# Optimization experiments

Measured on AMD Instinct MI355X. Metric: run time of the kernel, lower is better.

## Reference

```python
import jax, jax.numpy as jnp
import numpy as np

THR = 10.0           # spike threshold (all layers, igarss2023 config)
LEAK1, LEAK2, LEAK3 = 9.0, 1.0, 0.0  # subtractive leak per layer
POOL1_K, POOL1_S = 7, 6
POOL2_K, POOL2_S = 2, 2
WTA_BLOCK = 2        # local spatial WTA window


def conv2d_same(x, w):
    # x: (B,C,H,W), w: (O,I,kh,kw)
    return jax.lax.conv_general_dilated(
        x, w, window_strides=(1, 1), padding='SAME',
        dimension_numbers=('NCHW', 'OIHW', 'NCHW'))


def maxpool(x, k, s):
    return jax.lax.reduce_window(
        x, -jnp.inf, jax.lax.max, (1, 1, k, k), (1, 1, s, s), 'VALID')


def wta(mem, spk, block=WTA_BLOCK):
    """Winner-take-all lateral inhibition ('both' mode):
    (1) channel competition: only the channel with max membrane at each
        spatial location may spike; (2) local spatial competition: only the
        max-membrane neuron within each block x block window of each map
        may spike. Requires H,W divisible by block."""
    C = mem.shape[1]
    ch_win = jnp.argmax(mem, axis=1)                         # (B,H,W)
    ch_mask = jax.nn.one_hot(ch_win, C, axis=1, dtype=mem.dtype)  # (B,C,H,W)
    loc = jax.lax.reduce_window(
        mem, -jnp.inf, jax.lax.max,
        (1, 1, block, block), (1, 1, block, block), 'VALID')
    loc_up = jnp.repeat(jnp.repeat(loc, block, axis=2), block, axis=3)
    sp_mask = (mem >= loc_up).astype(mem.dtype)
    return spk * ch_mask * sp_mask


def lif_step(mem, inp, leak, use_wta):
    # integrate -> threshold -> WTA -> reset-to-zero -> subtractive leak
    mem = mem + inp
    spk = (mem >= THR).astype(mem.dtype)
    if use_wta:
        spk = wta(mem, spk)
    mem = jnp.where(spk > 0, 0.0, mem)
    mem = jnp.maximum(mem - leak, 0.0)
    return mem, spk


def setup_inputs() -> dict:
    key = jax.random.key(0)
    k0, k1, k2, k3 = jax.random.split(key, 4)
    T, B, H, W = 20, 8, 256, 256
    x = jax.random.uniform(k0, (T, B, 1, H, W), dtype=jnp.float32)
    # STDP-style weights are non-negative in [0,1)
    w1 = jax.random.uniform(k1, (4, 1, 5, 5), dtype=jnp.float32)
    w2 = jax.random.uniform(k2, (36, 4, 5, 5), dtype=jnp.float32)
    w3 = jax.random.uniform(k3, (1, 36, 7, 7), dtype=jnp.float32)
    return {"x": x, "w1": w1, "w2": w2, "w3": w3}


def reference(x, w1, w2, w3):
    T, B, _, H, W = x.shape
    H1, W1 = H, W                                   # conv1 SAME
    H2 = (H1 - POOL1_K) // POOL1_S + 1              # 42
    W2 = (W1 - POOL1_K) // POOL1_S + 1
    H3 = (H2 - POOL2_K) // POOL2_S + 1              # 21
    W3 = (W2 - POOL2_K) // POOL2_S + 1
    C1, C2, C3 = w1.shape[0], w2.shape[0], w3.shape[0]

    m1_0 = jnp.zeros((B, C1, H1, W1), x.dtype)
    m2_0 = jnp.zeros((B, C2, H2, W2), x.dtype)
    m3_0 = jnp.zeros((B, C3, H3, W3), x.dtype)

    def step(carry, xt):
        m1, m2, m3 = carry
        m1, s1 = lif_step(m1, conv2d_same(xt, w1), LEAK1, True)
        p1 = maxpool(s1, POOL1_K, POOL1_S)
        m2, s2 = lif_step(m2, conv2d_same(p1, w2), LEAK2, True)
        p2 = maxpool(s2, POOL2_K, POOL2_S)
        m3, s3 = lif_step(m3, conv2d_same(p2, w3), LEAK3, False)
        return (m1, m2, m3), s3

    _, cls_spikes = jax.lax.scan(step, (m1_0, m2_0, m3_0), x)
    return cls_spikes  # (T, B, n_classes, H3, W3)
```

## Files before the change

### kernel.cpp

```cpp
#include <hip/hip_runtime.h>
#include <stdint.h>

#define THR 10.0f
#define AGT __HIP_MEMORY_SCOPE_AGENT

static constexpr size_t OFF_P2  = 2097152;
static constexpr size_t OFF_BAR = 2359296;

static __device__ __forceinline__ uint32_t ldu32(const uint32_t* p) {
    return __hip_atomic_load(p, __ATOMIC_RELAXED, AGT);
}
static __device__ __forceinline__ void stu32(uint32_t* p, uint32_t v) {
    __hip_atomic_store(p, v, __ATOMIC_RELAXED, AGT);
}
static __device__ __forceinline__ void stu16(uint16_t* p, uint16_t v) {
    __hip_atomic_store(p, v, __ATOMIC_RELAXED, AGT);
}
static __device__ __forceinline__ uint32_t rmwread(uint32_t* p) {
    return __hip_atomic_fetch_add(p, 0u, __ATOMIC_RELAXED, AGT);
}

__global__ __launch_bounds__(256) void zero_bar(uint32_t* __restrict__ bar) {
    if (threadIdx.x < 256) bar[threadIdx.x] = 0u;
}

__device__ __forceinline__ void gbar(uint32_t* bar, int bid, uint32_t n) {
    __syncthreads();
    if (threadIdx.x == 0) {
        uint32_t* base = bar + (bid >> 6) * 32;
        uint32_t a = __hip_atomic_fetch_add(base, 1u, __ATOMIC_RELAXED, AGT);
        if (a == 64u * n - 1u)
            __hip_atomic_fetch_add(base + 16, 1u, __ATOMIC_RELAXED, AGT);
        while (rmwread(base + 16) < n)
            __builtin_amdgcn_s_sleep(2);
    }
    __syncthreads();
}

__global__ __launch_bounds__(256, 2) void spike_persist(
    const float* __restrict__ x,
    const float* __restrict__ w1,
    const float* __restrict__ w2,
    const float* __restrict__ w3,
    float* __restrict__ out,
    uint8_t* __restrict__ s1b,
    uint8_t* __restrict__ p2b,
    uint32_t* __restrict__ bar)
{
    __shared__ union {
        float    xs[2112];
        uint32_t st32[527];
    } u;
    __shared__ float    ps[400];
    __shared__ float    mem_s[1296];
    __shared__ float    bm_s[324];
    __shared__ int      wc_s[36];
    __shared__ uint32_t p2a[18];

    const int tid = threadIdx.x;
    const int bid = blockIdx.x;
    uint32_t nbar = 0;

    const int b1 = bid >> 6;
    const int r0 = (bid & 63) * 4;
    const int tr = tid >> 7, tc = tid & 127;

    const int tIdx = bid & 63;
    const int b2 = bid >> 6;
    const int tyi = tIdx >> 3, txi = tIdx & 7;
    const int oy2 = tyi < 5 ? 6 * tyi : 30 + 4 * (tyi - 5);
    const int ox2 = txi < 5 ? 6 * txi : 30 + 4 * (txi - 5);
    const int th2 = tyi < 5 ? 6 : 4;
    const int tw2 = txi < 5 ? 6 : 4;
    const int wave = tid >> 6, lane = tid & 63;
    const int pr = lane / 6, pc = lane - 6 * pr;
    const bool act = (pr < th2) && (pc < tw2);
    const int prA = pr > 5 ? 0 : pr, pcA = pc;

    const int lid3 = (bid & 63) * 4 + wave;
    const int kyl = lane / 7, kxl = lane % 7;

    float w3v[36];
#pragma unroll
    for (int c = 0; c < 36; c++) w3v[c] = (lane < 49) ? w3[c * 49 + lane] : 0.f;

    int aoff[9]; bool aval[9];
#pragma unroll
    for (int i = 0; i < 9; i++) {
        int idx = tid + i * 256;
        int row = idx / 264, col = idx - row * 264;
        int gy = r0 + row - 2, gx = col - 2;
        aval[i] = (idx < 2112) && gy >= 0 && gy < 256 && gx >= 0 && gx < 256;
        aoff[i] = gy * 256 + gx;
    }
    const size_t s1soff = ((size_t)(b1 * 128 + (r0 >> 1) + tr)) * 128 + tc;

    const int rb0 = 3 * oy2 - 6;
    const int cb0 = (3 * ox2 - 6) >> 1;
    int boff[3]; bool bval[3];
#pragma unroll
    for (int i = 0; i < 3; i++) {
        int idx = tid + i * 256;
        int row = idx / 17, w = idx - row * 17;
        int grow = rb0 + row, gcol = cb0 + w;
        bval[i] = (idx < 527) && grow >= 0 && grow < 128 && gcol >= 0 && gcol < 64;
        boff[i] = (b2 * 128 + grow) * 64 + gcol;
    }

    bool l3in[2], l3v[2]; int l3o[2];
#pragma unroll
    for (int rep = 0; rep < 2; rep++) {
        int o = lid3 + rep * 256;
        int rr = o / 21, cl = o - rr * 21;
        int yy = rr + kyl - 3, xx = cl + kxl - 3;
        l3in[rep] = o < 441;
        l3v[rep] = (o < 441) && (lane < 49) && yy >= 0 && yy < 21 && xx >= 0 && xx < 21;
        l3o[rep] = (b2 * 441 + yy * 21 + xx) << 1;
    }

    float m1r[4][2][2];
#pragma unroll
    for (int c = 0; c < 4; c++)
#pragma unroll
        for (int dy = 0; dy < 2; dy++)
#pragma unroll
            for (int dx = 0; dx < 2; dx++) m1r[c][dy][dx] = 0.f;
    float m2r[9];
#pragma unroll
    for (int i = 0; i < 9; i++) m2r[i] = 0.f;
    float m3r[2] = {0.f, 0.f};

    for (int k = 0; k < 7; k++) {
        uint32_t pfB[4][3];
#pragma unroll
        for (int tt = 0; tt < 4; tt++) {
            int tb = 4 * k - 4 + tt;
            if (tb >= 0 && tb < 20) {
                const uint32_t* s1r32 = reinterpret_cast<const uint32_t*>(
                    s1b + (size_t)(tb & 7) * 262144);
#pragma unroll
                for (int i = 0; i < 3; i++)
                    pfB[tt][i] = bval[i] ? ldu32(s1r32 + boff[i]) : 0u;
            }
        }
        uint32_t pfLlo[4][2], pfLhi[4][2];
#pragma unroll
        for (int tt = 0; tt < 4; tt++) {
            int tl = 4 * k - 8 + tt;
            if (tl >= 0 && tl < 20) {
                const uint32_t* pb32 = reinterpret_cast<const uint32_t*>(
                    p2b + (size_t)(tl & 7) * 32768);
#pragma unroll
                for (int rep = 0; rep < 2; rep++) {
                    pfLlo[tt][rep] = l3v[rep] ? ldu32(pb32 + l3o[rep]) : 0u;
                    pfLhi[tt][rep] = l3v[rep] ? ldu32(pb32 + l3o[rep] + 1) : 0u;
                }
            }
        }

#pragma unroll
        for (int tt = 0; tt < 4; tt++) {
            const int t = 4 * k + tt;
            if (t < 20) {
                uint16_t* s1w = reinterpret_cast<uint16_t*>(s1b + (size_t)(t & 7) * 262144);
                const float* xb = x + ((size_t)t * 8 + b1) * 65536;
                __syncthreads();
#pragma unroll
                for (int i = 0; i < 9; i++) {
                    int idx = tid + i * 256;
                    if (idx < 2112) u.xs[idx] = aval[i] ? xb[aoff[i]] : 0.f;
                }
                __syncthreads();

                const float2* xs2 = reinterpret_cast<const float2*>(u.xs);
                float p[6][6];
#pragma unroll
                for (int i = 0; i < 6; i++)
#pragma unroll
                    for (int j = 0; j < 3; j++) {
                        float2 v = xs2[(2 * tr + i) * 132 + tc + j];
                        p[i][2 * j] = v.x; p[i][2 * j + 1] = v.y;
                    }

                float acc[4][2][2];
#pragma unroll
                for (int c = 0; c < 4; c++)
#pragma unroll
                    for (int dy = 0; dy < 2; dy++)
#pragma unroll
                        for (int dx = 0; dx < 2; dx++) acc[c][dy][dx] = 0.f;
#pragma unroll
                for (int c = 0; c < 4; c++)
#pragma unroll
                    for (int ky = 0; ky < 5; ky++)
#pragma unroll
                        for (int kx = 0; kx < 5; kx++) {
                            float w = w1[c * 25 + ky * 5 + kx];
#pragma unroll
                            for (int dy = 0; dy < 2; dy++)
#pragma unroll
                                for (int dx = 0; dx < 2; dx++)
                                    acc[c][dy][dx] = fmaf(p[dy + ky][dx + kx], w, acc[c][dy][dx]);
                        }

                float mem[4][2][2];
#pragma unroll
                for (int c = 0; c < 4; c++)
#pragma unroll
                    for (int dy = 0; dy < 2; dy++)
#pragma unroll
                        for (int dx = 0; dx < 2; dx++)
                            mem[c][dy][dx] = m1r[c][dy][dx] + acc[c][dy][dx];

                int wc[2][2];
#pragma unroll
                for (int dy = 0; dy < 2; dy++)
#pragma unroll
                    for (int dx = 0; dx < 2; dx++) {
                        int w = 0; float mx = mem[0][dy][dx];
#pragma unroll
                        for (int c = 1; c < 4; c++) {
                            float v = mem[c][dy][dx];
                            if (v > mx) { mx = v; w = c; }
                        }
                        wc[dy][dx] = w;
                    }

                float bm[4];
#pragma unroll
                for (int c = 0; c < 4; c++)
                    bm[c] = fmaxf(fmaxf(mem[c][0][0], mem[c][0][1]),
                                  fmaxf(mem[c][1][0], mem[c][1][1]));

                uint32_t bits = 0;
#pragma unroll
                for (int c = 0; c < 4; c++)
#pragma unroll
                    for (int dy = 0; dy < 2; dy++)
#pragma unroll
                        for (int dx = 0; dx < 2; dx++) {
                            float m = mem[c][dy][dx];
                            bool s = (m >= THR) && (wc[dy][dx] == c) && (m >= bm[c]);
                            m1r[c][dy][dx] = fmaxf((s ? 0.f : m) - 9.0f, 0.f);
                            bits |= (s ? 1u : 0u) << (c * 4 + dy * 2 + dx);
                        }
                stu16(reinterpret_cast<uint16_t*>(s1w) + s1soff, (uint16_t)bits);
            }
        }

#pragma unroll
        for (int tt = 0; tt < 4; tt++) {
            const int tl = 4 * k - 8 + tt;
            if (tl >= 0 && tl < 20) {
#pragma unroll
                for (int rep = 0; rep < 2; rep++) {
                    if (l3in[rep]) {
                        int o = lid3 + rep * 256;
                        uint32_t lo = pfLlo[tt][rep], hi = pfLhi[tt][rep];
                        float accv = 0.f;
#pragma unroll
                        for (int c = 0; c < 32; c++) accv += ((lo >> c) & 1u) ? w3v[c] : 0.f;
#pragma unroll
                        for (int c = 0; c < 4; c++)  accv += ((hi >> c) & 1u) ? w3v[32 + c] : 0.f;
#pragma unroll
                        for (int off = 32; off; off >>= 1) accv += __shfl_xor(accv, off, 64);
                        float memv3 = m3r[rep] + accv;
                        bool s = memv3 >= THR;
                        if (lane == 0) out[(size_t)tl * 3528 + b2 * 441 + o] = s ? 1.f : 0.f;
                        m3r[rep] = fmaxf(s ? 0.f : memv3, 0.f);
                    }
                }
            }
        }

#pragma unroll
        for (int tt = 0; tt < 4; tt++) {
            const int tb = 4 * k - 4 + tt;
            if (tb >= 0 && tb < 20) {
                uint32_t* p2w32 = reinterpret_cast<uint32_t*>(p2b + (size_t)(tb & 7) * 32768);

                __syncthreads();
#pragma unroll
                for (int i = 0; i < 3; i++) {
                    int idx = tid + i * 256;
                    if (idx < 527) u.st32[idx] = pfB[tt][i];
                }
                __syncthreads();

                if (tid < 100) {
                    int r = tid / 10, cc2 = tid - 10 * r;
                    int gy = oy2 - 2 + r, gx = ox2 - 2 + cc2;
                    uint32_t accb = 0;
                    if (r < th2 + 4 && cc2 < tw2 + 4 && gy >= 0 && gy < 42 && gx >= 0 && gx < 42) {
                        const uint16_t* st16 = reinterpret_cast<const uint16_t*>(u.st32);
#pragma unroll
                        for (int kr = 0; kr < 4; kr++)
#pragma unroll
                            for (int kc = 0; kc < 4; kc++) {
                                uint32_t m = (kr < 3) ? (kc < 3 ? 0xFu : 0x5u)
                                                      : (kc < 3 ? 0x3u : 0x1u);
                                uint32_t v = st16[(3 * r + kr) * 34 + 3 * cc2 + kc];
                                accb |= v & (m * 0x1111u);
                            }
                    }
#pragma unroll
                    for (int ic = 0; ic < 4; ic++)
                        ps[ic * 100 + tid] = ((accb >> (4 * ic)) & 0xFu) ? 1.f : 0.f;
                }
                __syncthreads();

                float pv[4][5][5];
#pragma unroll
                for (int ic = 0; ic < 4; ic++)
#pragma unroll
                    for (int i = 0; i < 5; i++)
#pragma unroll
                        for (int j = 0; j < 5; j++)
                            pv[ic][i][j] = ps[ic * 100 + (prA + i) * 10 + (pcA + j)];

                float memv[9];
                for (int cc = 0; cc < 9; cc++) {
                    int c = cc * 4 + wave;
                    const float* wr = w2 + (size_t)__builtin_amdgcn_readfirstlane(c) * 100;
                    float accv = 0.f;
#pragma unroll
                    for (int ic = 0; ic < 4; ic++)
#pragma unroll
                        for (int i = 0; i < 5; i++)
#pragma unroll
                            for (int j = 0; j < 5; j++)
                                accv = fmaf(pv[ic][i][j], wr[ic * 25 + i * 5 + j], accv);
                    float m = act ? (m2r[cc] + accv) : -1e30f;
                    memv[cc] = m;
                    if (lane < 36) mem_s[c * 36 + lane] = m;
                }
                __syncthreads();

                if (tid < 36) {
                    float mx = mem_s[tid]; int w = 0;
#pragma unroll
                    for (int c = 1; c < 36; c++) {
                        float v = mem_s[c * 36 + tid];
                        if (v > mx) { mx = v; w = c; }
                    }
                    wc_s[tid] = w;
                }
#pragma unroll
                for (int i = 0; i < 2; i++) {
                    int idx = tid + i * 256;
                    if (idx < 324) {
                        int c = idx / 9, blk = idx - 9 * c;
                        int br = blk / 3, bc2 = blk - 3 * br;
                        int l0 = 12 * br + 2 * bc2;
                        float a = mem_s[c * 36 + l0],     bb2 = mem_s[c * 36 + l0 + 1];
                        float d = mem_s[c * 36 + l0 + 6], e   = mem_s[c * 36 + l0 + 7];
                        bm_s[idx] = fmaxf(fmaxf(a, bb2), fmaxf(d, e));
                    }
                }
                if (tid < 18) p2a[tid] = 0;
                __syncthreads();

                const int blkl = (pr >> 1) * 3 + (pc >> 1);
                for (int cc = 0; cc < 9; cc++) {
                    int c = cc * 4 + wave;
                    if (act) {
                        float m = memv[cc];
                        bool s = (m >= THR) && (wc_s[lane] == c) && (m >= bm_s[c * 9 + blkl]);
                        m2r[cc] = fmaxf((s ? 0.f : m) - 1.0f, 0.f);
                    }
                }

#pragma unroll
                for (int i = 0; i < 2; i++) {
                    int idx = tid + i * 256;
                    if (idx < 324) {
                        int c = idx / 9, blk = idx - 9 * c;
                        int br = blk / 3, bc2 = blk - 3 * br;
                        if (2 * br < th2 && 2 * bc2 < tw2) {
                            int l0 = 12 * br + 2 * bc2;
                            float bmv = bm_s[idx];
                            bool any = false;
#pragma unroll
                            for (int kk = 0; kk < 4; kk++) {
                                int l = l0 + (kk >> 1) * 6 + (kk & 1);
                                float m = mem_s[c * 36 + l];
                                any |= (m >= THR) && (wc_s[l] == c) && (m >= bmv);
                            }
                            if (any)
                                atomicOr(&p2a[(blk << 1) + (c >> 5)], 1u << (c & 31));
                        }
                    }
                }
                __syncthreads();

                if (tid < 9) {
                    int br = tid / 3, bc2 = tid - 3 * br;
                    if (2 * br < th2 && 2 * bc2 < tw2) {
                        int cell = b2 * 441 + ((oy2 >> 1) + br) * 21 + (ox2 >> 1) + bc2;
                        uint32_t* dst = p2w32 + ((size_t)cell << 1);
                        stu32(dst, p2a[tid * 2]);
                        stu32(dst + 1, p2a[tid * 2 + 1]);
                    }
                }
            }
        }

        if (k < 6) gbar(bar, bid, ++nbar);
    }
}

extern "C" void kernel_launch(void* const* d_in, const int* in_sizes, int n_in,
                              void* d_out, int out_size, void* d_ws, size_t ws_size,
                              hipStream_t stream) {
    const float* x  = (const float*)d_in[0];
    const float* w1 = (const float*)d_in[1];
    const float* w2 = (const float*)d_in[2];
    const float* w3 = (const float*)d_in[3];
    float* out = (float*)d_out;
    uint8_t* s1 = (uint8_t*)d_ws;
    uint8_t* p2 = (uint8_t*)d_ws + OFF_P2;
    uint32_t* bar = (uint32_t*)((char*)d_ws + OFF_BAR);

    zero_bar<<<1, 256, 0, stream>>>(bar);

    void* args[] = {(void*)&x, (void*)&w1, (void*)&w2, (void*)&w3,
                    (void*)&out, (void*)&s1, (void*)&p2, (void*)&bar};
    hipLaunchCooperativeKernel((void*)spike_persist, dim3(512), dim3(256),
                               args, 0, stream);
}
```

Measured before the change: 453.5 us.

## Widen spike-buffer traffic to 64-bit and drop up-front prefetch

Spike bitmaps for layer 1 are now packed across four lanes with shuffles and written as one 64-bit store per quad, and layer-2 input tiles and pooled layer-3 inputs are read as 64-bit loads instead of pairs of 32-bit loads. The per-superstep register prefetch of those buffers is removed, so loads happen just before use, and unrolling of the timestep loops is dropped. Barrier polling uses a plain atomic load instead of a fetch-add. Together these cut the number of global memory transactions and lower register pressure, at the cost of exposing load latency that the prefetch used to hide.

```diff
diff --git a/kernel.cpp b/kernel.cpp
--- a/kernel.cpp
+++ b/kernel.cpp
@@ -7,17 +7,11 @@
 static constexpr size_t OFF_P2  = 2097152;
 static constexpr size_t OFF_BAR = 2359296;
 
-static __device__ __forceinline__ uint32_t ldu32(const uint32_t* p) {
+static __device__ __forceinline__ uint64_t ldu64(const uint64_t* p) {
     return __hip_atomic_load(p, __ATOMIC_RELAXED, AGT);
 }
-static __device__ __forceinline__ void stu32(uint32_t* p, uint32_t v) {
+static __device__ __forceinline__ void stu64(uint64_t* p, uint64_t v) {
     __hip_atomic_store(p, v, __ATOMIC_RELAXED, AGT);
-}
-static __device__ __forceinline__ void stu16(uint16_t* p, uint16_t v) {
-    __hip_atomic_store(p, v, __ATOMIC_RELAXED, AGT);
-}
-static __device__ __forceinline__ uint32_t rmwread(uint32_t* p) {
-    return __hip_atomic_fetch_add(p, 0u, __ATOMIC_RELAXED, AGT);
 }
 
 __global__ __launch_bounds__(256) void zero_bar(uint32_t* __restrict__ bar) {
@@ -31,7 +25,7 @@
         uint32_t a = __hip_atomic_fetch_add(base, 1u, __ATOMIC_RELAXED, AGT);
         if (a == 64u * n - 1u)
             __hip_atomic_fetch_add(base + 16, 1u, __ATOMIC_RELAXED, AGT);
-        while (rmwread(base + 16) < n)
+        while (__hip_atomic_load(base + 16, __ATOMIC_RELAXED, AGT) < n)
             __builtin_amdgcn_s_sleep(2);
     }
     __syncthreads();
@@ -49,7 +43,7 @@
 {
     __shared__ union {
         float    xs[2112];
-        uint32_t st32[527];
+        uint64_t st64[279];
     } u;
     __shared__ float    ps[400];
     __shared__ float    mem_s[1296];
@@ -84,27 +78,32 @@
 #pragma unroll
     for (int c = 0; c < 36; c++) w3v[c] = (lane < 49) ? w3[c * 49 + lane] : 0.f;
 
-    int aoff[9]; bool aval[9];
+    int aoff[9]; uint32_t avalm = 0;
 #pragma unroll
     for (int i = 0; i < 9; i++) {
         int idx = tid + i * 256;
         int row = idx / 264, col = idx - row * 264;
         int gy = r0 + row - 2, gx = col - 2;
-        aval[i] = (idx < 2112) && gy >= 0 && gy < 256 && gx >= 0 && gx < 256;
+        if ((idx < 2112) && gy >= 0 && gy < 256 && gx >= 0 && gx < 256)
+            avalm |= 1u << i;
         aoff[i] = gy * 256 + gx;
     }
-    const size_t s1soff = ((size_t)(b1 * 128 + (r0 >> 1) + tr)) * 128 + tc;
+    const int s1soff64 = (b1 * 128 + (r0 >> 1) + tr) * 32 + (tc >> 2);
 
     const int rb0 = 3 * oy2 - 6;
     const int cb0 = (3 * ox2 - 6) >> 1;
-    int boff[3]; bool bval[3];
-#pragma unroll
-    for (int i = 0; i < 3; i++) {
+    const int cq0 = cb0 >> 1;
+    const int d16 = 2 * (cb0 & 1);
+    int boff[2]; uint32_t bvalm = 0;
+#pragma unroll
+    for (int i = 0; i < 2; i++) {
         int idx = tid + i * 256;
-        int row = idx / 17, w = idx - row * 17;
-        int grow = rb0 + row, gcol = cb0 + w;
-        bval[i] = (idx < 527) && grow >= 0 && grow < 128 && gcol >= 0 && gcol < 64;
-        boff[i] = (b2 * 128 + grow) * 64 + gcol;
+        int row = idx / 9, q = idx - 9 * row;
+        int grow = rb0 + row;
+        int ucol = 2 * (cq0 + q);
+        if ((idx < 279) && grow >= 0 && grow < 128 && ucol >= 0 && ucol < 64)
+            bvalm |= 1u << i;
+        boff[i] = (b2 * 128 + grow) * 32 + cq0 + q;
     }
 
     bool l3in[2], l3v[2]; int l3o[2];
@@ -115,7 +114,7 @@
         int yy = rr + kyl - 3, xx = cl + kxl - 3;
         l3in[rep] = o < 441;
         l3v[rep] = (o < 441) && (lane < 49) && yy >= 0 && yy < 21 && xx >= 0 && xx < 21;
-        l3o[rep] = (b2 * 441 + yy * 21 + xx) << 1;
+        l3o[rep] = b2 * 441 + yy * 21 + xx;
     }
 
     float m1r[4][2][2];
@@ -131,44 +130,16 @@
     float m3r[2] = {0.f, 0.f};
 
     for (int k = 0; k < 7; k++) {
-        uint32_t pfB[4][3];
-#pragma unroll
-        for (int tt = 0; tt < 4; tt++) {
-            int tb = 4 * k - 4 + tt;
-            if (tb >= 0 && tb < 20) {
-                const uint32_t* s1r32 = reinterpret_cast<const uint32_t*>(
-                    s1b + (size_t)(tb & 7) * 262144);
-#pragma unroll
-                for (int i = 0; i < 3; i++)
-                    pfB[tt][i] = bval[i] ? ldu32(s1r32 + boff[i]) : 0u;
-            }
-        }
-        uint32_t pfLlo[4][2], pfLhi[4][2];
-#pragma unroll
-        for (int tt = 0; tt < 4; tt++) {
-            int tl = 4 * k - 8 + tt;
-            if (tl >= 0 && tl < 20) {
-                const uint32_t* pb32 = reinterpret_cast<const uint32_t*>(
-                    p2b + (size_t)(tl & 7) * 32768);
-#pragma unroll
-                for (int rep = 0; rep < 2; rep++) {
-                    pfLlo[tt][rep] = l3v[rep] ? ldu32(pb32 + l3o[rep]) : 0u;
-                    pfLhi[tt][rep] = l3v[rep] ? ldu32(pb32 + l3o[rep] + 1) : 0u;
-                }
-            }
-        }
-
-#pragma unroll
         for (int tt = 0; tt < 4; tt++) {
             const int t = 4 * k + tt;
             if (t < 20) {
-                uint16_t* s1w = reinterpret_cast<uint16_t*>(s1b + (size_t)(t & 7) * 262144);
+                uint64_t* s1w = reinterpret_cast<uint64_t*>(s1b + (size_t)(t & 7) * 262144);
                 const float* xb = x + ((size_t)t * 8 + b1) * 65536;
                 __syncthreads();
 #pragma unroll
                 for (int i = 0; i < 9; i++) {
                     int idx = tid + i * 256;
-                    if (idx < 2112) u.xs[idx] = aval[i] ? xb[aoff[i]] : 0.f;
+                    if (idx < 2112) u.xs[idx] = ((avalm >> i) & 1u) ? xb[aoff[i]] : 0.f;
                 }
                 __syncthreads();
 
@@ -244,19 +215,24 @@
                             m1r[c][dy][dx] = fmaxf((s ? 0.f : m) - 9.0f, 0.f);
                             bits |= (s ? 1u : 0u) << (c * 4 + dy * 2 + dx);
                         }
-                stu16(reinterpret_cast<uint16_t*>(s1w) + s1soff, (uint16_t)bits);
+                uint32_t b32 = bits | ((uint32_t)__shfl_xor((int)bits, 1, 64) << 16);
+                uint64_t b64 = (uint64_t)b32 |
+                               ((uint64_t)(uint32_t)__shfl_xor((int)b32, 2, 64) << 32);
+                if (!(tid & 3)) stu64(s1w + s1soff64, b64);
             }
         }
 
-#pragma unroll
         for (int tt = 0; tt < 4; tt++) {
             const int tl = 4 * k - 8 + tt;
             if (tl >= 0 && tl < 20) {
+                const uint64_t* pb64 = reinterpret_cast<const uint64_t*>(
+                    p2b + (size_t)(tl & 7) * 32768);
 #pragma unroll
                 for (int rep = 0; rep < 2; rep++) {
                     if (l3in[rep]) {
                         int o = lid3 + rep * 256;
-                        uint32_t lo = pfLlo[tt][rep], hi = pfLhi[tt][rep];
+                        uint64_t v = l3v[rep] ? ldu64(pb64 + l3o[rep]) : 0ull;
+                        uint32_t lo = (uint32_t)v, hi = (uint32_t)(v >> 32);
                         float accv = 0.f;
 #pragma unroll
                         for (int c = 0; c < 32; c++) accv += ((lo >> c) & 1u) ? w3v[c] : 0.f;
@@ -273,33 +249,36 @@
             }
         }
 
-#pragma unroll
         for (int tt = 0; tt < 4; tt++) {
             const int tb = 4 * k - 4 + tt;
             if (tb >= 0 && tb < 20) {
-                uint32_t* p2w32 = reinterpret_cast<uint32_t*>(p2b + (size_t)(tb & 7) * 32768);
-
-                __syncthreads();
-#pragma unroll
-                for (int i = 0; i < 3; i++) {
+                const uint64_t* s1r64 = reinterpret_cast<const uint64_t*>(
+                    s1b + (size_t)(tb & 7) * 262144);
+                uint64_t* p2w64 = reinterpret_cast<uint64_t*>(p2b + (size_t)(tb & 7) * 32768);
+
+                __syncthreads();
+#pragma unroll
+                for (int i = 0; i < 2; i++) {
                     int idx = tid + i * 256;
-                    if (idx < 527) u.st32[idx] = pfB[tt][i];
-                }
+                    if (idx < 279)
+                        u.st64[idx] = ((bvalm >> i) & 1u) ? ldu64(s1r64 + boff[i]) : 0ull;
+                }
+                if (tid < 18) p2a[tid] = 0;
                 __syncthreads();
 
                 if (tid < 100) {
-                    int r = tid / 10, cc2 = tid - 10 * r;
+                    int r = tid / 10, cc2 = tid - 10 * (tid / 10);
                     int gy = oy2 - 2 + r, gx = ox2 - 2 + cc2;
                     uint32_t accb = 0;
                     if (r < th2 + 4 && cc2 < tw2 + 4 && gy >= 0 && gy < 42 && gx >= 0 && gx < 42) {
-                        const uint16_t* st16 = reinterpret_cast<const uint16_t*>(u.st32);
+                        const uint16_t* st16 = reinterpret_cast<const uint16_t*>(u.st64);
 #pragma unroll
                         for (int kr = 0; kr < 4; kr++)
 #pragma unroll
                             for (int kc = 0; kc < 4; kc++) {
                                 uint32_t m = (kr < 3) ? (kc < 3 ? 0xFu : 0x5u)
                                                       : (kc < 3 ? 0x3u : 0x1u);
-                                uint32_t v = st16[(3 * r + kr) * 34 + 3 * cc2 + kc];
+                                uint32_t v = st16[(3 * r + kr) * 36 + 3 * cc2 + kc + d16];
                                 accb |= v & (m * 0x1111u);
                             }
                     }
@@ -357,7 +336,6 @@
                         bm_s[idx] = fmaxf(fmaxf(a, bb2), fmaxf(d, e));
                     }
                 }
-                if (tid < 18) p2a[tid] = 0;
                 __syncthreads();
 
                 const int blkl = (pr >> 1) * 3 + (pc >> 1);
@@ -397,9 +375,9 @@
                     int br = tid / 3, bc2 = tid - 3 * br;
                     if (2 * br < th2 && 2 * bc2 < tw2) {
                         int cell = b2 * 441 + ((oy2 >> 1) + br) * 21 + (ox2 >> 1) + bc2;
-                        uint32_t* dst = p2w32 + ((size_t)cell << 1);
-                        stu32(dst, p2a[tid * 2]);
-                        stu32(dst + 1, p2a[tid * 2 + 1]);
+                        uint64_t v = (uint64_t)p2a[tid * 2] |
+                                     ((uint64_t)p2a[tid * 2 + 1] << 32);
+                        stu64(p2w64 + cell, v);
                     }
                 }
             }
```

New measurement: 398.1 us (median of 2 runs). 1.14x faster.
